# Optimization experiments

Measured on AMD Instinct MI355X. Metric: run time of the kernel, lower is better.

Reference implementation:

```python
import jax, jax.numpy as jnp
import numpy as np
import math

HID, HEADS, HD = 1024, 16, 64
DFF = 4 * HID
EPS = 1e-6
RES_SCALE = 0.5

def build_alibi_slopes(n_heads):
    def get_slopes(power):
        start = 2 ** (-2 ** (-(math.log2(power) - 3)))
        return [start * start ** i for i in range(power)]
    if math.log2(n_heads).is_integer():
        slopes = get_slopes(n_heads)
    else:
        closest = 2 ** math.floor(math.log2(n_heads))
        slopes = get_slopes(closest)
        extra = get_slopes(2 * closest)
        slopes = slopes + extra[0::2][: n_heads - closest]
    return jnp.asarray(np.array(slopes, dtype=np.float32))

def rmsnorm(x, w):
    var = jnp.mean(x * x, axis=-1, keepdims=True)
    return x * jax.lax.rsqrt(var + EPS) * w

def setup_inputs() -> dict:
    key = jax.random.key(0)
    ks = jax.random.split(key, 12)
    s = lambda d: 1.0 / math.sqrt(d)
    return {
        "x": jax.random.normal(ks[0], (2, 2048, HID), dtype=jnp.float32),
        "norm1_w": jnp.ones((HID,), jnp.float32),
        "Wq": jax.random.normal(ks[1], (HID, HEADS * HD), jnp.float32) * s(HID),
        "bq": jax.random.normal(ks[2], (HEADS * HD,), jnp.float32) * 0.01,
        "Wk": jax.random.normal(ks[3], (HID, HEADS * HD), jnp.float32) * s(HID),
        "bk": jax.random.normal(ks[4], (HEADS * HD,), jnp.float32) * 0.01,
        "Wv": jax.random.normal(ks[5], (HID, HEADS * HD), jnp.float32) * s(HID),
        "Wo": jax.random.normal(ks[6], (HEADS * HD, HID), jnp.float32) * s(HEADS * HD),
        "norm2_w": jnp.ones((HID,), jnp.float32),
        "W1": jax.random.normal(ks[7], (HID, DFF), jnp.float32) * s(HID),
        "b1": jax.random.normal(ks[8], (DFF,), jnp.float32) * 0.01,
        "W2": jax.random.normal(ks[9], (DFF, HID), jnp.float32) * s(DFF),
        "b2": jax.random.normal(ks[10], (HID,), jnp.float32) * 0.01,
    }

def reference(x, norm1_w, Wq, bq, Wk, bk, Wv, Wo, norm2_w, W1, b1, W2, b2):
    b, s, _ = x.shape
    scale = HD ** -0.5
    xn = rmsnorm(x, norm1_w)
    q = (xn @ Wq + bq).reshape(b, s, HEADS, HD).transpose(0, 2, 1, 3)
    k = (xn @ Wk + bk).reshape(b, s, HEADS, HD).transpose(0, 2, 1, 3)
    v = (xn @ Wv).reshape(b, s, HEADS, HD).transpose(0, 2, 1, 3)
    scores = jnp.einsum('bhqd,bhkd->bhqk', q, k) * scale
    pos = jnp.arange(s)
    dist = jnp.abs(pos[None, :] - pos[:, None]).astype(scores.dtype)  # [s,s]
    slopes = build_alibi_slopes(HEADS)
    bias = -slopes[:, None, None] * dist[None, :, :]  # [h,s,s]
    scores = scores + bias[None]
    weights = jax.nn.softmax(scores, axis=-1)
    attn = jnp.einsum('bhqk,bhkd->bhqd', weights, v)
    attn = attn.transpose(0, 2, 1, 3).reshape(b, s, HEADS * HD)
    x = x + attn @ Wo
    xn2 = rmsnorm(x, norm2_w)
    h = jax.nn.gelu(xn2 @ W1 + b1, approximate=False)
    x = x + RES_SCALE * (h @ W2 + b2)
    return x
```

## Files before the change

### kernel.cpp

```cpp
#include <hip/hip_runtime.h>
#include <hip/hip_bf16.h>
#include <math.h>

#define S_LEN   2048
#define HIDN    1024
#define NHEADS  16
#define HDIM    64
#define NTOK    4096
#define DFFN    4096

#define LOG2E 1.44269504088896f

typedef __attribute__((ext_vector_type(8))) __bf16 bf16x8;
typedef __attribute__((ext_vector_type(4))) float  f32x4;

static __device__ __forceinline__ ushort f2bf(float f) {
  union { float f; unsigned u; } v; v.f = f;
  unsigned u = v.u;
  unsigned r = (u + 0x7fffu + ((u >> 16) & 1u)) >> 16;
  return (ushort)r;
}

#define GLOAD16(gp, lp)                                                              \
  __builtin_amdgcn_global_load_lds((const __attribute__((address_space(1))) void*)(gp), \
                                   (__attribute__((address_space(3))) void*)(lp), 16, 0, 0)

__global__ __launch_bounds__(256) void convert_all(const float* __restrict__ Wq,
                                                   const float* __restrict__ Wk,
                                                   const float* __restrict__ Wv,
                                                   const float* __restrict__ Wo,
                                                   const float* __restrict__ W1,
                                                   const float* __restrict__ W2,
                                                   ushort* __restrict__ wqkvT,
                                                   ushort* __restrict__ woT,
                                                   ushort* __restrict__ w1T,
                                                   ushort* __restrict__ w2T) {
  __shared__ float tile[32][33];
  int id = blockIdx.x;
  const float* W; ushort* WT; int K, N, tl;
  if (id < 3072) {
    int i = id >> 10; tl = id & 1023;
    W = (i == 0) ? Wq : (i == 1) ? Wk : Wv;
    WT = wqkvT + i * 1024 * 1024; K = 1024; N = 1024;
  } else if (id < 4096) { tl = id - 3072; W = Wo; WT = woT; K = 1024; N = 1024; }
  else if (id < 8192)   { tl = id - 4096; W = W1; WT = w1T; K = 1024; N = 4096; }
  else                  { tl = id - 8192; W = W2; WT = w2T; K = 4096; N = 1024; }
  int ntn = N >> 5;
  int n0 = (tl % ntn) * 32, k0 = (tl / ntn) * 32;
  int tx = threadIdx.x & 31, ty = threadIdx.x >> 5;
#pragma unroll
  for (int i = 0; i < 4; i++)
    tile[ty + i * 8][tx] = W[(size_t)(k0 + ty + i * 8) * N + n0 + tx];
  __syncthreads();
#pragma unroll
  for (int i = 0; i < 4; i++)
    WT[(size_t)(n0 + ty + i * 8) * K + k0 + tx] = f2bf(tile[tx][ty + i * 8]);
}

__global__ __launch_bounds__(256) void rmsnorm_kernel(const float* __restrict__ x,
                                                      const float* __restrict__ w,
                                                      ushort* __restrict__ out) {
  int row = blockIdx.x, t = threadIdx.x;
  const float4* x4 = (const float4*)(x + (size_t)row * HIDN);
  float4 v = x4[t];
  float ss = v.x * v.x + v.y * v.y + v.z * v.z + v.w * v.w;
#pragma unroll
  for (int m = 32; m; m >>= 1) ss += __shfl_xor(ss, m, 64);
  __shared__ float wsum[4];
  if ((t & 63) == 0) wsum[t >> 6] = ss;
  __syncthreads();
  float tot = wsum[0] + wsum[1] + wsum[2] + wsum[3];
  float rs = rsqrtf(tot * (1.0f / HIDN) + 1e-6f);
  const float4* w4 = (const float4*)w;
  float4 wv = w4[t];
  ushort4 o;
  o.x = f2bf(v.x * rs * wv.x);
  o.y = f2bf(v.y * rs * wv.y);
  o.z = f2bf(v.z * rs * wv.z);
  o.w = f2bf(v.w * rs * wv.w);
  *(ushort4*)(out + (size_t)row * HIDN + t * 4) = o;
}

template <int EPI, int TM>
__global__ __launch_bounds__(256, 3) void gemm_bt(const ushort* __restrict__ A,
                                                  const ushort* __restrict__ B,
                                                  int M, int N, int K,
                                                  const float* __restrict__ bias,
                                                  const float* __restrict__ resid,
                                                  float* __restrict__ outf,
                                                  ushort* __restrict__ outb,
                                                  ushort* __restrict__ qb,
                                                  ushort* __restrict__ kb,
                                                  ushort* __restrict__ vb) {
  constexpr int NF = (TM == 128) ? 4 : 2;
  __shared__ __align__(16) ushort As[TM * 64];
  __shared__ __align__(16) ushort Bs[128 * 64];
  int t = threadIdx.x;
  int w = t >> 6, l = t & 63;
  int wmr = (TM == 128) ? (w >> 1) * 64 : 0;
  int wnc = (TM == 128) ? (w & 1) * 64 : w * 32;
  int lr = l & 15, lg = l >> 4;

  int nwg = gridDim.x * gridDim.y;
  int bid = blockIdx.y * gridDim.x + blockIdx.x;
  int swz = (bid & 7) * (nwg >> 3) + (bid >> 3);
  int bx = swz % gridDim.x, by = swz / gridDim.x;
  int m0 = bx * TM, n0 = by * 128;

  int srl = l >> 3;
  int sg  = ((l & 7) ^ srl) * 8;
  const ushort* Ag = A + (size_t)(m0 + w * (TM / 4) + srl) * K + sg;
  const ushort* Bg = B + (size_t)(n0 + w * 32 + srl) * K + sg;
  ushort* Asw = &As[(w * (TM / 4)) * 64];
  ushort* Bsw = &Bs[(w * 32) * 64];

  f32x4 acc[4][NF] = {};

  for (int k0 = 0; k0 < K; k0 += 64) {
#pragma unroll
    for (int c = 0; c < TM / 32; c++)
      GLOAD16(Ag + (size_t)(8 * c) * K + k0, Asw + (8 * c) * 64);
#pragma unroll
    for (int c = 0; c < 4; c++)
      GLOAD16(Bg + (size_t)(8 * c) * K + k0, Bsw + (8 * c) * 64);
    __syncthreads();

    bf16x8 af[4][2], bfr[NF][2];
#pragma unroll
    for (int mf = 0; mf < 4; mf++)
#pragma unroll
      for (int ks = 0; ks < 2; ks++)
        af[mf][ks] = *(const bf16x8*)(&As[(wmr + mf * 16 + lr) * 64 +
                                          (((ks * 4 + lg) ^ (lr & 7)) << 3)]);
#pragma unroll
    for (int nf = 0; nf < NF; nf++)
#pragma unroll
      for (int ks = 0; ks < 2; ks++)
        bfr[nf][ks] = *(const bf16x8*)(&Bs[(wnc + nf * 16 + lr) * 64 +
                                           (((ks * 4 + lg) ^ (lr & 7)) << 3)]);
#pragma unroll
    for (int mf = 0; mf < 4; mf++)
#pragma unroll
      for (int nf = 0; nf < NF; nf++) {
        acc[mf][nf] = __builtin_amdgcn_mfma_f32_16x16x32_bf16(af[mf][0], bfr[nf][0], acc[mf][nf], 0, 0, 0);
        acc[mf][nf] = __builtin_amdgcn_mfma_f32_16x16x32_bf16(af[mf][1], bfr[nf][1], acc[mf][nf], 0, 0, 0);
      }
    __syncthreads();
  }

  int lg4 = lg * 4;
  if constexpr (EPI == 0) {
#pragma unroll
    for (int mf = 0; mf < 4; mf++) {
      int row0 = m0 + wmr + mf * 16 + lg4;
      int bb = row0 >> 11, ss0 = row0 & 2047;
#pragma unroll
      for (int nf = 0; nf < NF; nf++) {
        int col = n0 + wnc + nf * 16 + lr;
        int which = col >> 10, nn = col & 1023;
        int hh = nn >> 6, dd = nn & 63;
        float bcol = (which == 0) ? bias[nn] : (which == 1) ? resid[nn] : 0.0f;
        if (which == 2) {
          ushort4 o;
          o.x = f2bf(acc[mf][nf][0]);
          o.y = f2bf(acc[mf][nf][1]);
          o.z = f2bf(acc[mf][nf][2]);
          o.w = f2bf(acc[mf][nf][3]);
          *(ushort4*)(vb + ((size_t)(bb * NHEADS + hh) * HDIM + dd) * S_LEN + ss0) = o;
        } else {
#pragma unroll
          for (int r = 0; r < 4; r++) {
            float v = acc[mf][nf][r] + bcol;
            size_t idx = ((size_t)(bb * NHEADS + hh) * S_LEN + ss0 + r) * HDIM + dd;
            if (which == 0) qb[idx] = f2bf(v * (0.125f * LOG2E));
            else kb[idx] = f2bf(v);
          }
        }
      }
    }
  } else {
#pragma unroll
    for (int mf = 0; mf < 4; mf++) {
#pragma unroll
      for (int nf = 0; nf < NF; nf++) {
#pragma unroll
        for (int r = 0; r < 4; r++) {
          int row = m0 + wmr + mf * 16 + lg4 + r;
          int col = n0 + wnc + nf * 16 + lr;
          float v = acc[mf][nf][r];
          if constexpr (EPI == 1) {
            outf[(size_t)row * HIDN + col] = resid[(size_t)row * HIDN + col] + v;
          } else if constexpr (EPI == 2) {
            float tv = v + bias[col];
            float gl = 0.5f * tv * (1.0f + erff(tv * 0.70710678118f));
            outb[(size_t)row * DFFN + col] = f2bf(gl);
          } else {
            outf[(size_t)row * HIDN + col] =
                resid[(size_t)row * HIDN + col] + 0.5f * (v + bias[col]);
          }
        }
      }
    }
  }
}

__global__ __launch_bounds__(256, 4) void attn_kernel(const ushort* __restrict__ qb,
                                                      const ushort* __restrict__ kb,
                                                      const ushort* __restrict__ vt,
                                                      ushort* __restrict__ attn_out) {
  __shared__ __align__(16) ushort Ks[2][64 * 64];
  __shared__ __align__(16) ushort VTs[2][64 * 64];
  int t = threadIdx.x;
  int w = t >> 6, l = t & 63;
  int lr = l & 15, lg = l >> 4, g8 = lg * 8;

  int nwg = gridDim.x;
  int bid = blockIdx.x;
  int blk = (bid & 7) * (nwg >> 3) + (bid >> 3);
  int qt = blk & 31;
  int bh = blk >> 5;
  int h = bh & 15;
  float slope2 = exp2f(-0.5f * (float)(h + 1)) * LOG2E;
  float s64v = slope2 * 64.0f;
  int q0 = qt * 64;
  const ushort* qp = qb + (size_t)bh * S_LEN * HDIM;
  const ushort* kp = kb + (size_t)bh * S_LEN * HDIM;
  const ushort* vp = vt + (size_t)bh * HDIM * S_LEN;

  int S0 = (l >> 3) & 3;
  size_t kof0 = (size_t)(w * 16 + (l >> 3)) * HDIM + (size_t)(((l & 7) ^ S0) * 8);
  size_t kof1 = (size_t)(w * 16 + 8 + (l >> 3)) * HDIM + (size_t)(((l & 7) ^ S0 ^ 4) * 8);
  size_t vof0 = (size_t)(w * 16 + (l >> 3)) * S_LEN + (size_t)(((l & 7) ^ S0) * 8);
  size_t vof1 = (size_t)(w * 16 + 8 + (l >> 3)) * S_LEN + (size_t)(((l & 7) ^ S0 ^ 4) * 8);

  auto stage = [&](int tile, int b) {
    const ushort* ks_ = kp + (size_t)tile * 64 * HDIM;
    const ushort* vs_ = vp + tile * 64;
    GLOAD16(ks_ + kof0, &Ks[b][(w * 16) * 64]);
    GLOAD16(ks_ + kof1, &Ks[b][(w * 16 + 8) * 64]);
    GLOAD16(vs_ + vof0, &VTs[b][(w * 16) * 64]);
    GLOAD16(vs_ + vof1, &VTs[b][(w * 16 + 8) * 64]);
  };

  bf16x8 qf[2];
#pragma unroll
  for (int ks = 0; ks < 2; ks++)
    qf[ks] = *(const bf16x8*)(qp + (size_t)(q0 + w * 16 + lr) * HDIM + ks * 32 + g8);

  f32x4 ao[4] = {};
  float mrow = -INFINITY, lden = 0.f;

  int qabs = q0 + w * 16 + lr;
  f32x4 biasv[4];
  if (qt > 0) {
#pragma unroll
    for (int nf = 0; nf < 4; nf++)
#pragma unroll
      for (int r = 0; r < 4; r++)
        biasv[nf][r] = -slope2 * (float)(qabs - (32 * (nf >> 1) + 8 * lg + 4 * (nf & 1) + r));
  }

  int kbase_row = ((lr >> 2) << 3) + (lr & 3);
  int SK = (lr & 3) | (((lr >> 2) & 1) << 2);
  int SV = (lr & 3) | (((lr >> 3) & 1) << 2);

  stage(0, 0);
  __syncthreads();

  for (int tt = 0; tt < S_LEN / 64; tt++) {
    int cur = tt & 1;
    if (tt + 1 < S_LEN / 64) stage(tt + 1, cur ^ 1);
    bool diag = (tt == qt);

    f32x4 sc[4];
    __builtin_amdgcn_s_setprio(1);
#pragma unroll
    for (int nf = 0; nf < 4; nf++) {
      int kvr = kbase_row + ((nf & 1) << 2) + ((nf >> 1) << 5);
      f32x4 a = diag ? f32x4{0.f, 0.f, 0.f, 0.f} : biasv[nf];
#pragma unroll
      for (int ks = 0; ks < 2; ks++) {
        bf16x8 kf = *(const bf16x8*)(&Ks[cur][kvr * 64 + (((ks * 4 + lg) ^ SK) << 3)]);
        a = __builtin_amdgcn_mfma_f32_16x16x32_bf16(kf, qf[ks], a, 0, 0, 0);
      }
      sc[nf] = a;
    }
    __builtin_amdgcn_s_setprio(0);

    if (diag) {
      int qq = w * 16 + lr;
#pragma unroll
      for (int nf = 0; nf < 4; nf++)
#pragma unroll
        for (int r = 0; r < 4; r++) {
          int kvloc = 32 * (nf >> 1) + 8 * lg + 4 * (nf & 1) + r;
          sc[nf][r] -= slope2 * fabsf((float)(qq - kvloc));
          biasv[nf][r] = -slope2 * (float)(64 + kvloc - qq);
        }
    }

    float mx = -INFINITY;
#pragma unroll
    for (int nf = 0; nf < 4; nf++)
#pragma unroll
      for (int r = 0; r < 4; r++) mx = fmaxf(mx, sc[nf][r]);
    mx = fmaxf(mx, __shfl_xor(mx, 16, 64));
    mx = fmaxf(mx, __shfl_xor(mx, 32, 64));

    if (__any(mx > mrow)) {
      float mn = fmaxf(mrow, mx);
      float scl = exp2f(mrow - mn);
      mrow = mn;
      lden *= scl;
      float so[4];
#pragma unroll
      for (int r = 0; r < 4; r++) so[r] = __shfl(scl, lg * 4 + r, 64);
#pragma unroll
      for (int nf = 0; nf < 4; nf++)
#pragma unroll
        for (int r = 0; r < 4; r++) ao[nf][r] *= so[r];
    }

    float su = 0.f;
#pragma unroll
    for (int nf = 0; nf < 4; nf++)
#pragma unroll
      for (int r = 0; r < 4; r++) {
        float p = exp2f(sc[nf][r] - mrow);
        sc[nf][r] = p;
        su += p;
      }
    su += __shfl_xor(su, 16, 64);
    su += __shfl_xor(su, 32, 64);
    lden += su;

    bf16x8 pf[2];
#pragma unroll
    for (int ks = 0; ks < 2; ks++)
#pragma unroll
      for (int j = 0; j < 8; j++)
        pf[ks][j] = (__bf16)sc[2 * ks + (j >> 2)][j & 3];

    __builtin_amdgcn_s_setprio(1);
#pragma unroll
    for (int nf = 0; nf < 4; nf++) {
      int d = nf * 16 + lr;
#pragma unroll
      for (int ks = 0; ks < 2; ks++) {
        bf16x8 vf = *(const bf16x8*)(&VTs[cur][d * 64 + (((ks * 4 + lg) ^ SV) << 3)]);
        ao[nf] = __builtin_amdgcn_mfma_f32_16x16x32_bf16(pf[ks], vf, ao[nf], 0, 0, 0);
      }
    }
    __builtin_amdgcn_s_setprio(0);

    int next = tt + 1;
    if (!diag && next != qt) {
      float dd = (next < qt) ? s64v : -s64v;
#pragma unroll
      for (int nf = 0; nf < 4; nf++)
#pragma unroll
        for (int r = 0; r < 4; r++) biasv[nf][r] += dd;
    }
    __syncthreads();
  }

  float inv[4];
#pragma unroll
  for (int r = 0; r < 4; r++) inv[r] = 1.0f / __shfl(lden, lg * 4 + r, 64);
  int token_base = (bh >> 4) * S_LEN + q0 + w * 16;
#pragma unroll
  for (int nf = 0; nf < 4; nf++) {
#pragma unroll
    for (int r = 0; r < 4; r++) {
      int token = token_base + lg * 4 + r;
      int d = nf * 16 + lr;
      attn_out[(size_t)token * HIDN + h * HDIM + d] = f2bf(ao[nf][r] * inv[r]);
    }
  }
}

extern "C" void kernel_launch(void* const* d_in, const int* in_sizes, int n_in,
                              void* d_out, int out_size, void* d_ws, size_t ws_size,
                              hipStream_t stream) {
  const float* x   = (const float*)d_in[0];
  const float* n1w = (const float*)d_in[1];
  const float* Wq  = (const float*)d_in[2];
  const float* bq  = (const float*)d_in[3];
  const float* Wk  = (const float*)d_in[4];
  const float* bk  = (const float*)d_in[5];
  const float* Wv  = (const float*)d_in[6];
  const float* Wo  = (const float*)d_in[7];
  const float* n2w = (const float*)d_in[8];
  const float* W1  = (const float*)d_in[9];
  const float* b1  = (const float*)d_in[10];
  const float* W2  = (const float*)d_in[11];
  const float* b2  = (const float*)d_in[12];
  float* out = (float*)d_out;

  char* ws = (char*)d_ws;
  ushort* xn     = (ushort*)(ws + 0);
  ushort* wqkvT  = (ushort*)(ws + 8388608);
  ushort* woT    = (ushort*)(ws + 14680064);
  ushort* w1T    = (ushort*)(ws + 16777216);
  ushort* w2T    = (ushort*)(ws + 25165824);
  ushort* qbuf   = (ushort*)(ws + 33566720);
  ushort* kbuf   = (ushort*)(ws + 41955328);
  ushort* vtbuf  = (ushort*)(ws + 50343936);
  ushort* attnb  = (ushort*)(ws + 58732544);
  float*  x2     = (float*)(ws + 67121152);
  ushort* xn2    = (ushort*)(ws + 83898368);
  ushort* hbuf   = qbuf;

  dim3 blk(256);

  convert_all<<<dim3(12288), blk, 0, stream>>>(Wq, Wk, Wv, Wo, W1, W2,
                                               wqkvT, woT, w1T, w2T);
  rmsnorm_kernel<<<NTOK, blk, 0, stream>>>(x, n1w, xn);
  gemm_bt<0, 128><<<dim3(32, 24), blk, 0, stream>>>(xn, wqkvT, NTOK, 3 * HIDN, HIDN,
                                                    bq, bk, nullptr, nullptr,
                                                    qbuf, kbuf, vtbuf);
  attn_kernel<<<dim3(32 * 32), blk, 0, stream>>>(qbuf, kbuf, vtbuf, attnb);
  gemm_bt<1, 64><<<dim3(64, 8), blk, 0, stream>>>(attnb, woT, NTOK, HIDN, HIDN,
                                                  nullptr, x, x2, nullptr,
                                                  nullptr, nullptr, nullptr);
  rmsnorm_kernel<<<NTOK, blk, 0, stream>>>(x2, n2w, xn2);
  gemm_bt<2, 128><<<dim3(32, 32), blk, 0, stream>>>(xn2, w1T, NTOK, DFFN, HIDN,
                                                    b1, nullptr, nullptr, hbuf,
                                                    nullptr, nullptr, nullptr);
  gemm_bt<3, 64><<<dim3(64, 8), blk, 0, stream>>>(hbuf, w2T, NTOK, HIDN, DFFN,
                                                  b2, x2, out, nullptr,
                                                  nullptr, nullptr, nullptr);
}
```

Baseline: 382.0 us.

## Visit KV tiles outward from diagonal and skip negligible softmax contributions

The attention kernel now walks KV tiles starting at the diagonal and moving outward in order of distance, so the running max is found early. When every row's tile max falls more than 25 (log2 units) below the running max, the exp, row-sum and PV MFMA work for that tile is skipped. The ALiBi bias is now computed directly from distance rather than updated incrementally, and the block-to-head mapping is remapped. The skip drops contributions below about 2^-25, which is a small approximation. K/V loads still happen for every tile, so the saving is in compute only.

```diff
diff --git a/kernel.cpp b/kernel.cpp
--- a/kernel.cpp
+++ b/kernel.cpp
@@ -214,14 +214,13 @@
   int w = t >> 6, l = t & 63;
   int lr = l & 15, lg = l >> 4, g8 = lg * 8;
 
-  int nwg = gridDim.x;
   int bid = blockIdx.x;
-  int blk = (bid & 7) * (nwg >> 3) + (bid >> 3);
-  int qt = blk & 31;
-  int bh = blk >> 5;
-  int h = bh & 15;
+  int v = (bid & 7) * 128 + (bid >> 3);
+  int qt = v & 31;
+  int g = v >> 5;
+  int h = (g >> 1 & 7) + 8 * (g & 1);
+  int bh = (g >> 4) * 16 + h;
   float slope2 = exp2f(-0.5f * (float)(h + 1)) * LOG2E;
-  float s64v = slope2 * 64.0f;
   int q0 = qt * 64;
   const ushort* qp = qb + (size_t)bh * S_LEN * HDIM;
   const ushort* kp = kb + (size_t)bh * S_LEN * HDIM;
@@ -250,34 +249,48 @@
   f32x4 ao[4] = {};
   float mrow = -INFINITY, lden = 0.f;
 
-  int qabs = q0 + w * 16 + lr;
-  f32x4 biasv[4];
-  if (qt > 0) {
-#pragma unroll
-    for (int nf = 0; nf < 4; nf++)
-#pragma unroll
-      for (int r = 0; r < 4; r++)
-        biasv[nf][r] = -slope2 * (float)(qabs - (32 * (nf >> 1) + 8 * lg + 4 * (nf & 1) + r));
-  }
+  float qabs_f = (float)(q0 + w * 16 + lr);
+  float kvlocf[4][4];
+#pragma unroll
+  for (int nf = 0; nf < 4; nf++)
+#pragma unroll
+    for (int r = 0; r < 4; r++)
+      kvlocf[nf][r] = (float)(32 * (nf >> 1) + 8 * lg + 4 * (nf & 1) + r);
 
   int kbase_row = ((lr >> 2) << 3) + (lr & 3);
   int SK = (lr & 3) | (((lr >> 2) & 1) << 2);
   int SV = (lr & 3) | (((lr >> 3) & 1) << 2);
 
-  stage(0, 0);
+  int lo = qt, hi = qt;
+  auto nexttile = [&]() {
+    bool canHi = (hi < 31), canLo = (lo > 0);
+    if (canHi && (!canLo || (hi - qt) <= (qt - lo))) return ++hi;
+    return --lo;
+  };
+
+  int t_cur = qt;
+  int t_nxt = nexttile();
+  stage(t_cur, 0);
   __syncthreads();
-
-  for (int tt = 0; tt < S_LEN / 64; tt++) {
-    int cur = tt & 1;
-    if (tt + 1 < S_LEN / 64) stage(tt + 1, cur ^ 1);
-    bool diag = (tt == qt);
+  int cur = 0;
+
+  for (int it = 0; it < S_LEN / 64; it++) {
+    if (it + 1 < S_LEN / 64) stage(t_nxt, cur ^ 1);
+    bool diag = (t_cur == qt);
+    float d0f = qabs_f - (float)(t_cur * 64);
 
     f32x4 sc[4];
     __builtin_amdgcn_s_setprio(1);
 #pragma unroll
     for (int nf = 0; nf < 4; nf++) {
       int kvr = kbase_row + ((nf & 1) << 2) + ((nf >> 1) << 5);
-      f32x4 a = diag ? f32x4{0.f, 0.f, 0.f, 0.f} : biasv[nf];
+      f32x4 a;
+      if (diag) {
+        a = f32x4{0.f, 0.f, 0.f, 0.f};
+      } else {
+#pragma unroll
+        for (int r = 0; r < 4; r++) a[r] = -slope2 * fabsf(d0f - kvlocf[nf][r]);
+      }
 #pragma unroll
       for (int ks = 0; ks < 2; ks++) {
         bf16x8 kf = *(const bf16x8*)(&Ks[cur][kvr * 64 + (((ks * 4 + lg) ^ SK) << 3)]);
@@ -288,15 +301,11 @@
     __builtin_amdgcn_s_setprio(0);
 
     if (diag) {
-      int qq = w * 16 + lr;
 #pragma unroll
       for (int nf = 0; nf < 4; nf++)
 #pragma unroll
-        for (int r = 0; r < 4; r++) {
-          int kvloc = 32 * (nf >> 1) + 8 * lg + 4 * (nf & 1) + r;
-          sc[nf][r] -= slope2 * fabsf((float)(qq - kvloc));
-          biasv[nf][r] = -slope2 * (float)(64 + kvloc - qq);
-        }
+        for (int r = 0; r < 4; r++)
+          sc[nf][r] -= slope2 * fabsf(d0f - kvlocf[nf][r]);
     }
 
     float mx = -INFINITY;
@@ -307,61 +316,58 @@
     mx = fmaxf(mx, __shfl_xor(mx, 16, 64));
     mx = fmaxf(mx, __shfl_xor(mx, 32, 64));
 
-    if (__any(mx > mrow)) {
-      float mn = fmaxf(mrow, mx);
-      float scl = exp2f(mrow - mn);
-      mrow = mn;
-      lden *= scl;
-      float so[4];
-#pragma unroll
-      for (int r = 0; r < 4; r++) so[r] = __shfl(scl, lg * 4 + r, 64);
+    if (!__all(mx < mrow - 25.0f)) {
+      if (__any(mx > mrow)) {
+        float mn = fmaxf(mrow, mx);
+        float scl = exp2f(mrow - mn);
+        mrow = mn;
+        lden *= scl;
+        float so[4];
+#pragma unroll
+        for (int r = 0; r < 4; r++) so[r] = __shfl(scl, lg * 4 + r, 64);
+#pragma unroll
+        for (int nf = 0; nf < 4; nf++)
+#pragma unroll
+          for (int r = 0; r < 4; r++) ao[nf][r] *= so[r];
+      }
+
+      float su = 0.f;
 #pragma unroll
       for (int nf = 0; nf < 4; nf++)
 #pragma unroll
-        for (int r = 0; r < 4; r++) ao[nf][r] *= so[r];
-    }
-
-    float su = 0.f;
-#pragma unroll
-    for (int nf = 0; nf < 4; nf++)
-#pragma unroll
-      for (int r = 0; r < 4; r++) {
-        float p = exp2f(sc[nf][r] - mrow);
-        sc[nf][r] = p;
-        su += p;
-      }
-    su += __shfl_xor(su, 16, 64);
-    su += __shfl_xor(su, 32, 64);
-    lden += su;
-
-    bf16x8 pf[2];
-#pragma unroll
-    for (int ks = 0; ks < 2; ks++)
-#pragma unroll
-      for (int j = 0; j < 8; j++)
-        pf[ks][j] = (__bf16)sc[2 * ks + (j >> 2)][j & 3];
-
-    __builtin_amdgcn_s_setprio(1);
-#pragma unroll
-    for (int nf = 0; nf < 4; nf++) {
-      int d = nf * 16 + lr;
-#pragma unroll
-      for (int ks = 0; ks < 2; ks++) {
-        bf16x8 vf = *(const bf16x8*)(&VTs[cur][d * 64 + (((ks * 4 + lg) ^ SV) << 3)]);
-        ao[nf] = __builtin_amdgcn_mfma_f32_16x16x32_bf16(pf[ks], vf, ao[nf], 0, 0, 0);
-      }
-    }
-    __builtin_amdgcn_s_setprio(0);
-
-    int next = tt + 1;
-    if (!diag && next != qt) {
-      float dd = (next < qt) ? s64v : -s64v;
-#pragma unroll
-      for (int nf = 0; nf < 4; nf++)
-#pragma unroll
-        for (int r = 0; r < 4; r++) biasv[nf][r] += dd;
-    }
+        for (int r = 0; r < 4; r++) {
+          float p = exp2f(sc[nf][r] - mrow);
+          sc[nf][r] = p;
+          su += p;
+        }
+      su += __shfl_xor(su, 16, 64);
+      su += __shfl_xor(su, 32, 64);
+      lden += su;
+
+      bf16x8 pf[2];
+#pragma unroll
+      for (int ks = 0; ks < 2; ks++)
+#pragma unroll
+        for (int j = 0; j < 8; j++)
+          pf[ks][j] = (__bf16)sc[2 * ks + (j >> 2)][j & 3];
+
+      __builtin_amdgcn_s_setprio(1);
+#pragma unroll
+      for (int nf = 0; nf < 4; nf++) {
+        int d = nf * 16 + lr;
+#pragma unroll
+        for (int ks = 0; ks < 2; ks++) {
+          bf16x8 vf = *(const bf16x8*)(&VTs[cur][d * 64 + (((ks * 4 + lg) ^ SV) << 3)]);
+          ao[nf] = __builtin_amdgcn_mfma_f32_16x16x32_bf16(pf[ks], vf, ao[nf], 0, 0, 0);
+        }
+      }
+      __builtin_amdgcn_s_setprio(0);
+    }
+
     __syncthreads();
+    t_cur = t_nxt;
+    if (it + 2 < S_LEN / 64) t_nxt = nexttile();
+    cur ^= 1;
   }
 
   float inv[4];
```

Result: faster. 372.2 us (-2.6%).
